# Kernel optimization log

Measured on AMD Instinct MI355X. Metric: run time of the kernel, lower is better.

Reference implementation:

```python
import jax, jax.numpy as jnp
import numpy as np

B, H, W, C = 8, 64, 64, 512
DQK = C // 8  # query/key channel dim from Conv2D(filters//8, 1)


def setup_inputs() -> dict:
    key = jax.random.key(0)
    ks = jax.random.split(key, 8)
    s_in = 1.0 / np.sqrt(C)
    x = jax.random.normal(ks[0], (B, H, W, C), dtype=jnp.float32)
    Wq = jax.random.normal(ks[1], (C, DQK), dtype=jnp.float32) * s_in
    bq = jnp.zeros((DQK,), dtype=jnp.float32)
    Wk = jax.random.normal(ks[2], (C, DQK), dtype=jnp.float32) * s_in
    bk = jnp.zeros((DQK,), dtype=jnp.float32)
    Wv = jax.random.normal(ks[3], (C, C), dtype=jnp.float32) * s_in
    bv = jnp.zeros((C,), dtype=jnp.float32)
    # gamma initialized to zeros in the original, but use a nonzero value so
    # the attention branch actually contributes to the output/gradients.
    gamma = jnp.ones((1,), dtype=jnp.float32) * 0.5
    return {"x": x, "Wq": Wq, "bq": bq, "Wk": Wk, "bk": bk,
            "Wv": Wv, "bv": bv, "gamma": gamma}


def reference(x, Wq, bq, Wk, bk, Wv, bv, gamma):
    b, h, w, c = x.shape
    n = h * w  # spatial_size
    xf = x.reshape(b, n, c)
    # 1x1 convs == per-pixel channel matmuls
    q = xf @ Wq + bq            # [B, N, C//8]
    k = xf @ Wk + bk            # [B, N, C//8]
    v = xf @ Wv + bv            # [B, N, C]
    # Dot(axes=-1): attn[b,i,j] = sum_d q[b,i,d] * k[b,j,d]
    attn = jnp.einsum('bid,bjd->bij', q, k)
    attn = jax.nn.softmax(attn, axis=-1)
    # Dot(axes=-2): out[b,j,c] = sum_i attn[b,i,j] * v[b,i,c]  (note transpose)
    out = jnp.einsum('bij,bic->bjc', attn, v)
    out = out.reshape(b, h, w, c)
    return gamma * out + x
```

## Files before the change

kernel.cpp:

```cpp
#include <hip/hip_runtime.h>
#include <hip/hip_bf16.h>
#include <cstdio>

typedef unsigned short u16;
typedef __attribute__((ext_vector_type(4))) float f32x4;
typedef __attribute__((ext_vector_type(8))) short s16x8;

__device__ __forceinline__ u16 bf16b(float f) {
  union { float f; unsigned u; } c; c.f = f;
  unsigned u = c.u;
  return (u16)((u + 0x7FFFu + ((u >> 16) & 1u)) >> 16);
}

__device__ __forceinline__ void load16(const void* g, void* l) {
  __builtin_amdgcn_global_load_lds(
      (const __attribute__((address_space(1))) void*)g,
      (__attribute__((address_space(3))) void*)l, 16, 0, 0);
}

#define BARV() asm volatile("s_waitcnt vmcnt(0) lgkmcnt(0)\n\ts_barrier" ::: "memory")
#define BAR() asm volatile("s_waitcnt lgkmcnt(0)\n\ts_barrier" ::: "memory")


__global__ __launch_bounds__(256) void cvt_x_k(const float* __restrict__ x,
                                               u16* __restrict__ xb) {
  long i = ((long)blockIdx.x * 256 + threadIdx.x) * 4;
  float4 f = *(const float4*)&x[i];
  unsigned lo = (unsigned)bf16b(f.x) | ((unsigned)bf16b(f.y) << 16);
  unsigned hi = (unsigned)bf16b(f.z) | ((unsigned)bf16b(f.w) << 16);
  uint2 v; v.x = lo; v.y = hi;
  *(uint2*)&xb[i] = v;
}

__global__ __launch_bounds__(256) void cvt_w_k(const float* __restrict__ Wq,
                                               const float* __restrict__ Wk,
                                               const float* __restrict__ Wv,
                                               u16* __restrict__ Wcat) {
  int idx = blockIdx.x * 256 + threadIdx.x;
  int nn = idx >> 9, k = idx & 511;
  float v;
  if (nn < 64)       v = Wq[k * 64 + nn];
  else if (nn < 128) v = Wk[k * 64 + (nn - 64)];
  else               v = Wv[k * 512 + (nn - 128)];
  Wcat[idx] = bf16b(v);
}

__global__ __launch_bounds__(256, 2) void projGemm(
    const u16* __restrict__ A, const u16* __restrict__ B,
    u16* __restrict__ Qb, u16* __restrict__ Kb, u16* __restrict__ Vt,
    const float* __restrict__ bq, const float* __restrict__ bk,
    const float* __restrict__ bv) {
  constexpr int BM = 128, BN = 128, FM = 4, FN = 4;
  __shared__ __align__(16) u16 At[BM * 64];
  __shared__ __align__(16) u16 Bt[BN * 64];
  const int tid = threadIdx.x;
  const int lane = tid & 63, w = tid >> 6;
  const int wr = w >> 1, wc = w & 1;
  const int l15 = lane & 15, lhi = lane >> 4;
  const long m0 = (long)blockIdx.x * BM;
  const long n0 = (long)blockIdx.y * BN;

  f32x4 acc[FM][FN] = {};

  for (int k0 = 0; k0 < 512; k0 += 64) {
#pragma unroll
    for (int it = 0; it < 8; ++it) {
      int q = it * 256 + tid;
      if (q < BM * 8) {
        int row = q >> 3, c8 = q & 7;
        load16(A + (m0 + row) * 512 + k0 + c8 * 8, &At[q * 8]);
      } else {
        int q2 = q - BM * 8;
        int row = q2 >> 3, c8 = q2 & 7;
        load16(B + (n0 + row) * 512 + k0 + c8 * 8, &Bt[q2 * 8]);
      }
    }
    __syncthreads();
#pragma unroll
    for (int kk = 0; kk < 64; kk += 32) {
      s16x8 af[FM], bf[FN];
#pragma unroll
      for (int i = 0; i < FM; ++i)
        af[i] = *(const s16x8*)&At[(wr * 64 + i * 16 + l15) * 64 + kk + lhi * 8];
#pragma unroll
      for (int j = 0; j < FN; ++j)
        bf[j] = *(const s16x8*)&Bt[(wc * 64 + j * 16 + l15) * 64 + kk + lhi * 8];
#pragma unroll
      for (int i = 0; i < FM; ++i)
#pragma unroll
        for (int j = 0; j < FN; ++j)
          acc[i][j] = __builtin_amdgcn_mfma_f32_16x16x32_bf16(af[i], bf[j],
                                                              acc[i][j], 0, 0, 0);
    }
    __syncthreads();
  }

#pragma unroll
  for (int i = 0; i < FM; ++i) {
#pragma unroll
    for (int j = 0; j < FN; ++j) {
      long mm = m0 + wr * 64 + i * 16 + lhi * 4;
      long nn = n0 + wc * 64 + j * 16 + l15;
      if (nn < 64) {
        float bb = bq[nn];
#pragma unroll
        for (int r = 0; r < 4; ++r)
          Qb[(mm + r) * 64 + nn] = bf16b(acc[i][j][r] + bb);
      } else if (nn < 128) {
        float bb = bk[nn - 64];
#pragma unroll
        for (int r = 0; r < 4; ++r)
          Kb[(mm + r) * 64 + nn - 64] = bf16b(acc[i][j][r] + bb);
      } else {
        long c = nn - 128;
        float bb = bv[c];
        unsigned u01 = (unsigned)bf16b(acc[i][j][0] + bb) |
                       ((unsigned)bf16b(acc[i][j][1] + bb) << 16);
        unsigned u23 = (unsigned)bf16b(acc[i][j][2] + bb) |
                       ((unsigned)bf16b(acc[i][j][3] + bb) << 16);
        uint2 u; u.x = u01; u.y = u23;
        *(uint2*)&Vt[(mm >> 12) * 512 * 4096 + c * 4096 + (mm & 4095)] = u;
      }
    }
  }
}

__global__ __launch_bounds__(256, 2) void stats_k(const u16* __restrict__ Qb,
                                                  const u16* __restrict__ Kb,
                                                  float* __restrict__ m_part,
                                                  float* __restrict__ l_part) {
  const int b = blockIdx.z, jc = blockIdx.y;
  const long i0 = (long)blockIdx.x * 128;
  const u16* Q = Qb + (long)b * 4096 * 64;
  const u16* Kp = Kb + (long)b * 4096 * 64;
  __shared__ __align__(16) u16 Qt[128 * 64];
  __shared__ __align__(16) u16 Kt[128 * 64];
  const int tid = threadIdx.x, lane = tid & 63, w = tid >> 6;
  const int l15 = lane & 15, lhi = lane >> 4;

#pragma unroll
  for (int it = 0; it < 4; ++it) {
    int q = it * 256 + tid;
    int row = q >> 3, c8 = q & 7;
    load16(Q + (i0 + row) * 64 + c8 * 8, &Qt[q * 8]);
  }

  float mrun[2][4], lrun[2][4];
#pragma unroll
  for (int i = 0; i < 2; ++i)
#pragma unroll
    for (int r = 0; r < 4; ++r) { mrun[i][r] = -1e30f; lrun[i][r] = 0.f; }

  for (int jt = 0; jt < 8; ++jt) {
    long j0 = (long)jc * 1024 + jt * 128;
#pragma unroll
    for (int it = 0; it < 4; ++it) {
      int q = it * 256 + tid;
      int row = q >> 3, c8 = q & 7;
      load16(Kp + (j0 + row) * 64 + c8 * 8, &Kt[q * 8]);
    }
    __syncthreads();
    f32x4 acc[2][8] = {};
#pragma unroll
    for (int kk = 0; kk < 64; kk += 32) {
      s16x8 af[2], bf[8];
#pragma unroll
      for (int i = 0; i < 2; ++i)
        af[i] = *(const s16x8*)&Qt[(w * 32 + i * 16 + l15) * 64 + kk + lhi * 8];
#pragma unroll
      for (int j = 0; j < 8; ++j)
        bf[j] = *(const s16x8*)&Kt[(j * 16 + l15) * 64 + kk + lhi * 8];
#pragma unroll
      for (int i = 0; i < 2; ++i)
#pragma unroll
        for (int j = 0; j < 8; ++j)
          acc[i][j] = __builtin_amdgcn_mfma_f32_16x16x32_bf16(af[i], bf[j],
                                                              acc[i][j], 0, 0, 0);
    }
#pragma unroll
    for (int i = 0; i < 2; ++i)
#pragma unroll
      for (int r = 0; r < 4; ++r) {
        float tm = acc[i][0][r];
#pragma unroll
        for (int j = 1; j < 8; ++j) tm = fmaxf(tm, acc[i][j][r]);
        float mo = mrun[i][r];
        float mn = fmaxf(mo, tm);
        float s = 0.f;
#pragma unroll
        for (int j = 0; j < 8; ++j) s += __expf(acc[i][j][r] - mn);
        lrun[i][r] = lrun[i][r] * __expf(mo - mn) + s;
        mrun[i][r] = mn;
      }
    __syncthreads();
  }

#pragma unroll
  for (int i = 0; i < 2; ++i)
#pragma unroll
    for (int r = 0; r < 4; ++r) {
      float m = mrun[i][r], l = lrun[i][r];
#pragma unroll
      for (int d = 1; d < 16; d <<= 1) {
        float mo = __shfl_xor(m, d);
        float lo = __shfl_xor(l, d);
        float mn = fmaxf(m, mo);
        l = l * __expf(m - mn) + lo * __expf(mo - mn);
        m = mn;
      }
      if (l15 == 0) {
        long ig = i0 + w * 32 + i * 16 + lhi * 4 + r;
        long idx = ((long)(b * 4 + jc)) * 4096 + ig;
        m_part[idx] = m;
        l_part[idx] = l;
      }
    }
}

__global__ __launch_bounds__(256) void merge_k(const float* __restrict__ m_part,
                                               const float* __restrict__ l_part,
                                               float* __restrict__ mfin,
                                               float* __restrict__ linv) {
  int idx = blockIdx.x * 256 + threadIdx.x;
  int b = idx >> 12, i = idx & 4095;
  float m = -1e30f, l = 0.f;
#pragma unroll
  for (int jc = 0; jc < 4; ++jc) {
    long o = ((long)(b * 4 + jc)) * 4096 + i;
    float mp = m_part[o], lp = l_part[o];
    float mn = fmaxf(m, mp);
    l = l * __expf(m - mn) + lp * __expf(mp - mn);
    m = mn;
  }
  mfin[idx] = m;
  linv[idx] = 1.0f / l;
}

__global__ __launch_bounds__(512, 2) void fusedPV(
    const u16* __restrict__ Qb, const u16* __restrict__ Kb,
    const u16* __restrict__ Vt, const float* __restrict__ mfin,
    const float* __restrict__ lnv, const float* __restrict__ x,
    const float* __restrict__ gamma, float* __restrict__ out) {
  __shared__ __align__(16) u16 Kt[256 * 64];
  __shared__ __align__(16) u16 Qc[2][64 * 64];
  __shared__ __align__(16) u16 Vc[2][256 * 64];
  __shared__ __align__(16) u16 Pl[256 * 64];
  const int tid = threadIdx.x, lane = tid & 63, w = tid >> 6;
  const int l15 = lane & 15, lhi = lane >> 4;
  const int wi = w & 1, wj = w >> 1, wc = w & 1;
  const int b = blockIdx.z;
  const long j0 = (long)blockIdx.x * 256;
  const long c0 = (long)blockIdx.y * 256;
  const u16* Qg = Qb + (long)b * 4096 * 64;
  const u16* Kg = Kb + (long)b * 4096 * 64;
  const u16* Vg = Vt + (long)b * 512 * 4096;
  const float* mg = mfin + (long)b * 4096;
  const float* lg = lnv + (long)b * 4096;

#pragma unroll
  for (int p = 0; p < 4; ++p) {
    int s = p * 512 + tid;
    int r = s >> 3, col = s & 7, cg = col ^ (r & 7);
    load16(Kg + (j0 + r) * 64 + cg * 8, (char*)Kt + r * 128 + col * 16);
  }
  {
    int r = tid >> 3, col = tid & 7, cg = col ^ (r & 7);
    load16(Qg + (long)r * 64 + cg * 8, (char*)&Qc[0][0] + r * 128 + col * 16);
#pragma unroll
    for (int p = 0; p < 4; ++p) {
      int s = p * 512 + tid;
      int r2 = s >> 3, c2 = s & 7, cg2 = c2 ^ (r2 & 7);
      load16(Vg + (c0 + r2) * 4096 + cg2 * 8,
             (char*)&Vc[0][0] + r2 * 128 + c2 * 16);
    }
  }

  f32x4 acc2[4][8] = {};
  const float gma = gamma[0];
  int cur = 0;

  for (int t = 0; t < 64; ++t) {
    const int i_base = t * 64;
    BARV();
    if (t < 63) {
      const long ib2 = (long)(t + 1) * 64;
      int r = tid >> 3, col = tid & 7, cg = col ^ (r & 7);
      load16(Qg + (ib2 + r) * 64 + cg * 8,
             (char*)&Qc[cur ^ 1][0] + r * 128 + col * 16);
#pragma unroll
      for (int p = 0; p < 4; ++p) {
        int s = p * 512 + tid;
        int r2 = s >> 3, c2 = s & 7, cg2 = c2 ^ (r2 & 7);
        load16(Vg + (c0 + r2) * 4096 + ib2 + cg2 * 8,
               (char*)&Vc[cur ^ 1][0] + r2 * 128 + c2 * 16);
      }
    }

    f32x4 acc1[2][4] = {};
#pragma unroll
    for (int kk = 0; kk < 64; kk += 32) {
      s16x8 af[2], bk4[4];
#pragma unroll
      for (int fi = 0; fi < 2; ++fi) {
        int r = wi * 32 + fi * 16 + l15;
        af[fi] = *(const s16x8*)((const char*)&Qc[cur][0] + r * 128 +
                                 (((kk + lhi * 8) * 2) ^ ((r & 7) << 4)));
      }
#pragma unroll
      for (int fj = 0; fj < 4; ++fj) {
        int r = wj * 64 + fj * 16 + l15;
        bk4[fj] = *(const s16x8*)((const char*)Kt + r * 128 +
                                  (((kk + lhi * 8) * 2) ^ ((r & 7) << 4)));
      }
#pragma unroll
      for (int fi = 0; fi < 2; ++fi)
#pragma unroll
        for (int fj = 0; fj < 4; ++fj)
          acc1[fi][fj] = __builtin_amdgcn_mfma_f32_16x16x32_bf16(
              af[fi], bk4[fj], acc1[fi][fj], 0, 0, 0);
    }

#pragma unroll
    for (int fi = 0; fi < 2; ++fi) {
      int i0l = wi * 32 + fi * 16 + lhi * 4;
      f32x4 mv = *(const f32x4*)&mg[i_base + i0l];
      f32x4 lv = *(const f32x4*)&lg[i_base + i0l];
#pragma unroll
      for (int fj = 0; fj < 4; ++fj) {
        int j = wj * 64 + fj * 16 + l15;
        float p0 = __expf(acc1[fi][fj][0] - mv[0]) * lv[0];
        float p1 = __expf(acc1[fi][fj][1] - mv[1]) * lv[1];
        float p2 = __expf(acc1[fi][fj][2] - mv[2]) * lv[2];
        float p3 = __expf(acc1[fi][fj][3] - mv[3]) * lv[3];
        unsigned u01 = (unsigned)bf16b(p0) | ((unsigned)bf16b(p1) << 16);
        unsigned u23 = (unsigned)bf16b(p2) | ((unsigned)bf16b(p3) << 16);
        char* base = (char*)Pl + j * 128;
        int byt = (i0l * 2) ^ ((j & 7) << 4);
        *(unsigned*)(base + byt) = u01;
        *(unsigned*)(base + byt + 4) = u23;
      }
    }
    BAR();

#pragma unroll
    for (int kk = 0; kk < 64; kk += 32) {
      s16x8 pa[4];
#pragma unroll
      for (int fm = 0; fm < 4; ++fm) {
        int r = wj * 64 + fm * 16 + l15;
        pa[fm] = *(const s16x8*)((const char*)Pl + r * 128 +
                                 (((kk + lhi * 8) * 2) ^ ((r & 7) << 4)));
      }
#pragma unroll
      for (int fn = 0; fn < 8; ++fn) {
        int r = wc * 128 + fn * 16 + l15;
        s16x8 vb = *(const s16x8*)((const char*)&Vc[cur][0] + r * 128 +
                                   (((kk + lhi * 8) * 2) ^ ((r & 7) << 4)));
#pragma unroll
        for (int fm = 0; fm < 4; ++fm)
          acc2[fm][fn] = __builtin_amdgcn_mfma_f32_16x16x32_bf16(
              pa[fm], vb, acc2[fm][fn], 0, 0, 0);
      }
    }
    cur ^= 1;
  }

#pragma unroll
  for (int fm = 0; fm < 4; ++fm) {
#pragma unroll
    for (int fn = 0; fn < 8; ++fn) {
      long j = j0 + wj * 64 + fm * 16 + lhi * 4;
      long c = c0 + wc * 128 + fn * 16 + l15;
#pragma unroll
      for (int r = 0; r < 4; ++r) {
        long o = ((long)b * 4096 + j + r) * 512 + c;
        out[o] = gma * acc2[fm][fn][r] + x[o];
      }
    }
  }
}


extern "C" void kernel_launch(void* const* d_in, const int* in_sizes, int n_in,
                              void* d_out, int out_size, void* d_ws,
                              size_t ws_size, hipStream_t stream) {
  const float* x = (const float*)d_in[0];
  const float* Wq = (const float*)d_in[1];
  const float* bq = (const float*)d_in[2];
  const float* Wk = (const float*)d_in[3];
  const float* bk = (const float*)d_in[4];
  const float* Wv = (const float*)d_in[5];
  const float* bv = (const float*)d_in[6];
  const float* gamma = (const float*)d_in[7];
  float* out = (float*)d_out;

  char* ws = (char*)d_ws;
  size_t off = 0;
  auto alloc = [&](size_t bytes) {
    char* p = ws + off;
    off += (bytes + 255) & ~(size_t)255;
    return p;
  };
  u16* xb = (u16*)alloc((size_t)32768 * 512 * 2);
  u16* Wcat = (u16*)alloc((size_t)640 * 512 * 2);
  u16* Qb = (u16*)alloc((size_t)8 * 4096 * 64 * 2);
  u16* Kb = (u16*)alloc((size_t)8 * 4096 * 64 * 2);
  u16* Vt = (u16*)alloc((size_t)8 * 512 * 4096 * 2);
  float* m_part = (float*)alloc((size_t)8 * 4 * 4096 * 4);
  float* l_part = (float*)alloc((size_t)8 * 4 * 4096 * 4);
  float* mfin = (float*)alloc((size_t)8 * 4096 * 4);
  float* lnv = (float*)alloc((size_t)8 * 4096 * 4);
  if (off > ws_size) {
    fprintf(stderr, "kernel_launch: ws too small: need %zu have %zu\n", off,
            ws_size);
    return;
  }

  cvt_w_k<<<1280, 256, 0, stream>>>(Wq, Wk, Wv, Wcat);
  cvt_x_k<<<16384, 256, 0, stream>>>(x, xb);
  projGemm<<<dim3(256, 5, 1), 256, 0, stream>>>(xb, Wcat, Qb, Kb, Vt, bq, bk,
                                                bv);
  stats_k<<<dim3(32, 4, 8), 256, 0, stream>>>(Qb, Kb, m_part, l_part);
  merge_k<<<128, 256, 0, stream>>>(m_part, l_part, mfin, lnv);
  fusedPV<<<dim3(16, 2, 8), 512, 0, stream>>>(Qb, Kb, Vt, mfin, lnv, x,
                                              gamma, out);
}
```

Baseline: 314.4 us.

## Merge conversion kernels, keep K fragments in registers, remap fusedPV block order

```diff
diff --git a/kernel.cpp b/kernel.cpp
--- a/kernel.cpp
+++ b/kernel.cpp
@@ -22,27 +22,29 @@
 #define BAR() asm volatile("s_waitcnt lgkmcnt(0)\n\ts_barrier" ::: "memory")
 
 
-__global__ __launch_bounds__(256) void cvt_x_k(const float* __restrict__ x,
-                                               u16* __restrict__ xb) {
-  long i = ((long)blockIdx.x * 256 + threadIdx.x) * 4;
-  float4 f = *(const float4*)&x[i];
-  unsigned lo = (unsigned)bf16b(f.x) | ((unsigned)bf16b(f.y) << 16);
-  unsigned hi = (unsigned)bf16b(f.z) | ((unsigned)bf16b(f.w) << 16);
-  uint2 v; v.x = lo; v.y = hi;
-  *(uint2*)&xb[i] = v;
-}
-
-__global__ __launch_bounds__(256) void cvt_w_k(const float* __restrict__ Wq,
-                                               const float* __restrict__ Wk,
-                                               const float* __restrict__ Wv,
-                                               u16* __restrict__ Wcat) {
-  int idx = blockIdx.x * 256 + threadIdx.x;
-  int nn = idx >> 9, k = idx & 511;
-  float v;
-  if (nn < 64)       v = Wq[k * 64 + nn];
-  else if (nn < 128) v = Wk[k * 64 + (nn - 64)];
-  else               v = Wv[k * 512 + (nn - 128)];
-  Wcat[idx] = bf16b(v);
+__global__ __launch_bounds__(256) void cvt_all_k(const float* __restrict__ x,
+                                                 const float* __restrict__ Wq,
+                                                 const float* __restrict__ Wk,
+                                                 const float* __restrict__ Wv,
+                                                 u16* __restrict__ xb,
+                                                 u16* __restrict__ Wcat) {
+  int bid = blockIdx.x;
+  if (bid < 16384) {
+    long i = ((long)bid * 256 + threadIdx.x) * 4;
+    float4 f = *(const float4*)&x[i];
+    unsigned lo = (unsigned)bf16b(f.x) | ((unsigned)bf16b(f.y) << 16);
+    unsigned hi = (unsigned)bf16b(f.z) | ((unsigned)bf16b(f.w) << 16);
+    uint2 v; v.x = lo; v.y = hi;
+    *(uint2*)&xb[i] = v;
+  } else {
+    int idx = (bid - 16384) * 256 + threadIdx.x;
+    int nn = idx >> 9, k = idx & 511;
+    float v;
+    if (nn < 64)       v = Wq[k * 64 + nn];
+    else if (nn < 128) v = Wk[k * 64 + (nn - 64)];
+    else               v = Wv[k * 512 + (nn - 128)];
+    Wcat[idx] = bf16b(v);
+  }
 }
 
 __global__ __launch_bounds__(256, 2) void projGemm(
@@ -241,16 +243,17 @@
     const u16* __restrict__ Vt, const float* __restrict__ mfin,
     const float* __restrict__ lnv, const float* __restrict__ x,
     const float* __restrict__ gamma, float* __restrict__ out) {
-  __shared__ __align__(16) u16 Kt[256 * 64];
   __shared__ __align__(16) u16 Qc[2][64 * 64];
   __shared__ __align__(16) u16 Vc[2][256 * 64];
   __shared__ __align__(16) u16 Pl[256 * 64];
   const int tid = threadIdx.x, lane = tid & 63, w = tid >> 6;
   const int l15 = lane & 15, lhi = lane >> 4;
   const int wi = w & 1, wj = w >> 1, wc = w & 1;
-  const int b = blockIdx.z;
-  const long j0 = (long)blockIdx.x * 256;
-  const long c0 = (long)blockIdx.y * 256;
+  const int s = blockIdx.x + 16 * (blockIdx.y + 2 * blockIdx.z);
+  const int pi = (s & 7) * 32 + (s >> 3);
+  const int b = pi >> 5;
+  const long j0 = (long)(pi & 15) * 256;
+  const long c0 = (long)((pi >> 4) & 1) * 256;
   const u16* Qg = Qb + (long)b * 4096 * 64;
   const u16* Kg = Kb + (long)b * 4096 * 64;
   const u16* Vg = Vt + (long)b * 512 * 4096;
@@ -259,17 +262,29 @@
 
 #pragma unroll
   for (int p = 0; p < 4; ++p) {
-    int s = p * 512 + tid;
-    int r = s >> 3, col = s & 7, cg = col ^ (r & 7);
-    load16(Kg + (j0 + r) * 64 + cg * 8, (char*)Kt + r * 128 + col * 16);
-  }
+    int q = p * 512 + tid;
+    int r = q >> 3, col = q & 7, cg = col ^ (r & 7);
+    load16(Kg + (j0 + r) * 64 + cg * 8, (char*)Pl + r * 128 + col * 16);
+  }
+  BARV();
+  s16x8 kf[4][2];
+#pragma unroll
+  for (int fj = 0; fj < 4; ++fj)
+#pragma unroll
+    for (int kx = 0; kx < 2; ++kx) {
+      int r = wj * 64 + fj * 16 + l15;
+      kf[fj][kx] = *(const s16x8*)((const char*)Pl + r * 128 +
+                                   (((kx * 32 + lhi * 8) * 2) ^ ((r & 7) << 4)));
+    }
+  __syncthreads();
+
   {
     int r = tid >> 3, col = tid & 7, cg = col ^ (r & 7);
     load16(Qg + (long)r * 64 + cg * 8, (char*)&Qc[0][0] + r * 128 + col * 16);
 #pragma unroll
     for (int p = 0; p < 4; ++p) {
-      int s = p * 512 + tid;
-      int r2 = s >> 3, c2 = s & 7, cg2 = c2 ^ (r2 & 7);
+      int q = p * 512 + tid;
+      int r2 = q >> 3, c2 = q & 7, cg2 = c2 ^ (r2 & 7);
       load16(Vg + (c0 + r2) * 4096 + cg2 * 8,
              (char*)&Vc[0][0] + r2 * 128 + c2 * 16);
     }
@@ -289,8 +304,8 @@
              (char*)&Qc[cur ^ 1][0] + r * 128 + col * 16);
 #pragma unroll
       for (int p = 0; p < 4; ++p) {
-        int s = p * 512 + tid;
-        int r2 = s >> 3, c2 = s & 7, cg2 = c2 ^ (r2 & 7);
+        int q = p * 512 + tid;
+        int r2 = q >> 3, c2 = q & 7, cg2 = c2 ^ (r2 & 7);
         load16(Vg + (c0 + r2) * 4096 + ib2 + cg2 * 8,
                (char*)&Vc[cur ^ 1][0] + r2 * 128 + c2 * 16);
       }
@@ -298,26 +313,20 @@
 
     f32x4 acc1[2][4] = {};
 #pragma unroll
-    for (int kk = 0; kk < 64; kk += 32) {
-      s16x8 af[2], bk4[4];
+    for (int kx = 0; kx < 2; ++kx) {
+      s16x8 af[2];
 #pragma unroll
       for (int fi = 0; fi < 2; ++fi) {
         int r = wi * 32 + fi * 16 + l15;
         af[fi] = *(const s16x8*)((const char*)&Qc[cur][0] + r * 128 +
-                                 (((kk + lhi * 8) * 2) ^ ((r & 7) << 4)));
-      }
-#pragma unroll
-      for (int fj = 0; fj < 4; ++fj) {
-        int r = wj * 64 + fj * 16 + l15;
-        bk4[fj] = *(const s16x8*)((const char*)Kt + r * 128 +
-                                  (((kk + lhi * 8) * 2) ^ ((r & 7) << 4)));
+                                 (((kx * 32 + lhi * 8) * 2) ^ ((r & 7) << 4)));
       }
 #pragma unroll
       for (int fi = 0; fi < 2; ++fi)
 #pragma unroll
         for (int fj = 0; fj < 4; ++fj)
           acc1[fi][fj] = __builtin_amdgcn_mfma_f32_16x16x32_bf16(
-              af[fi], bk4[fj], acc1[fi][fj], 0, 0, 0);
+              af[fi], kf[fj][kx], acc1[fi][fj], 0, 0, 0);
     }
 
 #pragma unroll
@@ -343,7 +352,8 @@
     BAR();
 
 #pragma unroll
-    for (int kk = 0; kk < 64; kk += 32) {
+    for (int kx = 0; kx < 2; ++kx) {
+      int kk = kx * 32;
       s16x8 pa[4];
 #pragma unroll
       for (int fm = 0; fm < 4; ++fm) {
@@ -416,8 +426,7 @@
     return;
   }
 
-  cvt_w_k<<<1280, 256, 0, stream>>>(Wq, Wk, Wv, Wcat);
-  cvt_x_k<<<16384, 256, 0, stream>>>(x, xb);
+  cvt_all_k<<<16384 + 1280, 256, 0, stream>>>(x, Wq, Wk, Wv, xb, Wcat);
   projGemm<<<dim3(256, 5, 1), 256, 0, stream>>>(xb, Wcat, Qb, Kb, Vt, bq, bk,
                                                 bv);
   stats_k<<<dim3(32, 4, 8), 256, 0, stream>>>(Qb, Kb, m_part, l_part);
```

After: 324.0 us. +3.1%, slower.
